# Kernel tuning notes

Measured on AMD Instinct MI355X. Metric: run time of the kernel, lower is better.

The kernel has to match this reference:

```python
import jax, jax.numpy as jnp
import numpy as np

H = 4      # heads
C = 32     # out channels per head (hidden_channels)
G = 64     # num graphs


def transformer_conv(x, src, dst, Wq, bq, Wk, bk, Wv, bv, Ws, bs):
    # PyG TransformerConv, concat=False, root_weight=True, beta=False.
    N = x.shape[0]
    q = (x @ Wq + bq).reshape(N, H, C)
    k = (x @ Wk + bk).reshape(N, H, C)
    v = (x @ Wv + bv).reshape(N, H, C)
    qe = q[dst]            # [E,H,C] gather target queries
    ke = k[src]            # [E,H,C] gather source keys
    ve = v[src]            # [E,H,C] gather source values
    alpha = (qe * ke).sum(-1) / jnp.sqrt(jnp.asarray(C, x.dtype))  # [E,H]
    amax = jax.ops.segment_max(alpha, dst, num_segments=N)          # [N,H]
    a = jnp.exp(alpha - amax[dst])
    denom = jax.ops.segment_sum(a, dst, num_segments=N)             # [N,H]
    a = a / (denom[dst] + 1e-16)
    out = jax.ops.segment_sum(ve * a[..., None], dst, num_segments=N)  # [N,H,C]
    out = out.mean(axis=1)          # concat=False -> head average
    return out + x @ Ws + bs        # root skip


def setup_inputs() -> dict:
    key = jax.random.key(0)
    ks = jax.random.split(key, 24)
    N, E, Fin = 40000, 640000, 128
    x = jax.random.normal(ks[0], (N, Fin), dtype=jnp.float32)
    edge_index = jax.random.randint(ks[1], (2, E), 0, N, dtype=jnp.int64)
    batch = jnp.sort(jax.random.randint(ks[2], (N,), 0, G, dtype=jnp.int64))
    s = 0.05
    w = lambda k, shp: jax.random.normal(k, shp, dtype=jnp.float32) * s
    d = {"x": x, "edge_index": edge_index, "batch": batch,
         "Wq1": w(ks[3], (Fin, H * C)), "bq1": w(ks[4], (H * C,)),
         "Wk1": w(ks[5], (Fin, H * C)), "bk1": w(ks[6], (H * C,)),
         "Wv1": w(ks[7], (Fin, H * C)), "bv1": w(ks[8], (H * C,)),
         "Ws1": w(ks[9], (Fin, C)), "bs1": w(ks[10], (C,)),
         "Wq2": w(ks[11], (C, H * C)), "bq2": w(ks[12], (H * C,)),
         "Wk2": w(ks[13], (C, H * C)), "bk2": w(ks[14], (H * C,)),
         "Wv2": w(ks[15], (C, H * C)), "bv2": w(ks[16], (H * C,)),
         "Ws2": w(ks[17], (C, C)), "bs2": w(ks[18], (C,)),
         "Wlin": w(ks[19], (C, 16)), "blin": w(ks[20], (16,))}
    return d


def reference(x, edge_index, batch,
              Wq1, bq1, Wk1, bk1, Wv1, bv1, Ws1, bs1,
              Wq2, bq2, Wk2, bk2, Wv2, bv2, Ws2, bs2,
              Wlin, blin):
    src, dst = edge_index[0], edge_index[1]
    h = transformer_conv(x, src, dst, Wq1, bq1, Wk1, bk1, Wv1, bv1, Ws1, bs1)
    h = jax.nn.relu(h)
    h = transformer_conv(h, src, dst, Wq2, bq2, Wk2, bk2, Wv2, bv2, Ws2, bs2)
    # global mean pool over graphs
    sums = jax.ops.segment_sum(h, batch, num_segments=G)                  # [G,C]
    cnts = jax.ops.segment_sum(jnp.ones((h.shape[0],), h.dtype), batch, num_segments=G)
    pooled = sums / jnp.maximum(cnts, 1.0)[:, None]
    return pooled @ Wlin + blin
```

## Files before the change

### kernel.cpp

```cpp
#include <hip/hip_runtime.h>
#include <hip/hip_bf16.h>
#include <hip/hip_fp16.h>
#include <math.h>

#define HH 4
#define CC 32
#define HC 128
#define GG 64

typedef _Float16 f16x2 __attribute__((ext_vector_type(2)));
typedef _Float16 f16x8 __attribute__((ext_vector_type(8)));
typedef float f32x4 __attribute__((ext_vector_type(4)));

__device__ __forceinline__ f16x2 u2h(unsigned u) {
    union { unsigned u; f16x2 h; } x; x.u = u; return x.h;
}
__device__ __forceinline__ unsigned pkh(float a, float b) {
    __half2 h = __floats2half2_rn(a, b);
    union { __half2 h; unsigned u; } x; x.h = h; return x.u;
}
__device__ __forceinline__ f16x8 uq2h8(uint4 u) {
    union { uint4 u; f16x8 h; } x; x.u = u; return x.h;
}

__device__ __forceinline__ void wfrag_item(const float* __restrict__ Wq, const float* __restrict__ Wk,
    const float* __restrict__ Wv, const float* __restrict__ Ws,
    uint4* __restrict__ wfrag, int KS, int idx)
{
    int lane = idx & 63;
    int t = idx >> 6;
    int ks = t % KS, ct = t / KS;
    int r = lane & 15, g = lane >> 4;
    const float* W; int c, stride;
    if (ct < 8)       { W = Wq; c = ct * 16 + r;        stride = HC; }
    else if (ct < 16) { W = Wk; c = (ct - 8) * 16 + r;  stride = HC; }
    else if (ct < 24) { W = Wv; c = (ct - 16) * 16 + r; stride = HC; }
    else              { W = Ws; c = (ct - 24) * 16 + r; stride = CC; }
    unsigned u[4];
    #pragma unroll
    for (int jj = 0; jj < 4; ++jj) {
        int k = ks * 32 + g * 8 + jj * 2;
        u[jj] = pkh(W[(size_t)k * stride + c], W[(size_t)(k + 1) * stride + c]);
    }
    wfrag[idx] = make_uint4(u[0], u[1], u[2], u[3]);
}

__global__ void prep_kernel(const float* __restrict__ x, unsigned* __restrict__ xh, int n4,
    const float* __restrict__ Wq1, const float* __restrict__ Wk1,
    const float* __restrict__ Wv1, const float* __restrict__ Ws1, uint4* __restrict__ wfrag1,
    const float* __restrict__ Wq2, const float* __restrict__ Wk2,
    const float* __restrict__ Wv2, const float* __restrict__ Ws2, uint4* __restrict__ wfrag2,
    int* __restrict__ deg, int N, float* __restrict__ sums)
{
    const int N1 = 26 * 4 * 64;
    const int N2 = 26 * 1 * 64;
    int i = blockIdx.x * 256 + threadIdx.x;
    if (i < n4) {
        float4 f = ((const float4*)x)[i];
        ((uint2*)xh)[i] = make_uint2(pkh(f.x, f.y), pkh(f.z, f.w));
        return;
    }
    i -= n4;
    if (i < N1) { wfrag_item(Wq1, Wk1, Wv1, Ws1, wfrag1, 4, i); return; }
    i -= N1;
    if (i < N2) { wfrag_item(Wq2, Wk2, Wv2, Ws2, wfrag2, 1, i); return; }
    i -= N2;
    if (i < N) { deg[i] = 0; return; }
    i -= N;
    if (i < GG * CC + GG) sums[i] = 0.f;
}

template<int KDIM>
__global__ __launch_bounds__(256) void qkv_mfma_kernel(
    const ushort* __restrict__ xh, const uint4* __restrict__ wfrag,
    const float* __restrict__ bq, const float* __restrict__ bk,
    const float* __restrict__ bv, const float* __restrict__ bs,
    unsigned* __restrict__ qh, uint4* __restrict__ kv4, float* __restrict__ skip,
    int N)
{
    constexpr int KS = KDIM / 32;
    const int lane = threadIdx.x & 63;
    const int wv = threadIdx.x >> 6;
    const int n0 = (blockIdx.x * 4 + wv) * 16;
    if (n0 >= N) return;
    const int r = lane & 15, g = lane >> 4;
    const int node = n0 + r;

    f16x8 a[KS];
    #pragma unroll
    for (int ks = 0; ks < KS; ++ks)
        a[ks] = uq2h8(*(const uint4*)&xh[(size_t)node * KDIM + ks * 32 + g * 8]);

    if (blockIdx.y == 0) {
        const float SC2 = 0.25500526806584186f;
        f32x4 acc[10];
        #pragma unroll
        for (int i = 0; i < 10; ++i) acc[i] = (f32x4){0.f, 0.f, 0.f, 0.f};
        #pragma unroll
        for (int i = 0; i < 8; ++i)
            #pragma unroll
            for (int ks = 0; ks < KS; ++ks) {
                f16x8 w = uq2h8(wfrag[((size_t)i * KS + ks) * 64 + lane]);
                acc[i] = __builtin_amdgcn_mfma_f32_16x16x32_f16(w, a[ks], acc[i], 0, 0, 0);
            }
        #pragma unroll
        for (int i = 0; i < 2; ++i)
            #pragma unroll
            for (int ks = 0; ks < KS; ++ks) {
                f16x8 w = uq2h8(wfrag[((size_t)(24 + i) * KS + ks) * 64 + lane]);
                acc[8 + i] = __builtin_amdgcn_mfma_f32_16x16x32_f16(w, a[ks], acc[8 + i], 0, 0, 0);
            }
        if (node < N) {
            #pragma unroll
            for (int i = 0; i < 8; ++i) {
                float4 bb = *(const float4*)&bq[i * 16 + g * 4];
                uint2 o = make_uint2(pkh((acc[i][0] + bb.x) * SC2, (acc[i][1] + bb.y) * SC2),
                                     pkh((acc[i][2] + bb.z) * SC2, (acc[i][3] + bb.w) * SC2));
                *(uint2*)&qh[(size_t)node * 64 + i * 8 + g * 2] = o;
            }
            #pragma unroll
            for (int i = 0; i < 2; ++i) {
                float4 bb = *(const float4*)&bs[i * 16 + g * 4];
                float4 o = make_float4(acc[8 + i][0] + bb.x, acc[8 + i][1] + bb.y,
                                       acc[8 + i][2] + bb.z, acc[8 + i][3] + bb.w);
                *(float4*)&skip[(size_t)node * CC + i * 16 + g * 4] = o;
            }
        }
    } else {
        f32x4 acck[8], accv[8];
        #pragma unroll
        for (int i = 0; i < 8; ++i) { acck[i] = (f32x4){0.f,0.f,0.f,0.f}; accv[i] = (f32x4){0.f,0.f,0.f,0.f}; }
        #pragma unroll
        for (int i = 0; i < 8; ++i)
            #pragma unroll
            for (int ks = 0; ks < KS; ++ks) {
                f16x8 wk = uq2h8(wfrag[((size_t)(8 + i) * KS + ks) * 64 + lane]);
                acck[i] = __builtin_amdgcn_mfma_f32_16x16x32_f16(wk, a[ks], acck[i], 0, 0, 0);
                f16x8 wvf = uq2h8(wfrag[((size_t)(16 + i) * KS + ks) * 64 + lane]);
                accv[i] = __builtin_amdgcn_mfma_f32_16x16x32_f16(wvf, a[ks], accv[i], 0, 0, 0);
            }
        if (node < N) {
            #pragma unroll
            for (int i = 0; i < 8; ++i) {
                float4 bbk = *(const float4*)&bk[i * 16 + g * 4];
                float4 bbv = *(const float4*)&bv[i * 16 + g * 4];
                uint4 o;
                o.x = pkh(acck[i][0] + bbk.x, acck[i][1] + bbk.y);
                o.y = pkh(acck[i][2] + bbk.z, acck[i][3] + bbk.w);
                o.z = pkh(accv[i][0] + bbv.x, accv[i][1] + bbv.y);
                o.w = pkh(accv[i][2] + bbv.z, accv[i][3] + bbv.w);
                kv4[(size_t)node * 32 + i * 4 + g] = o;
            }
        }
    }
}

__global__ void deg_kernel(const int* __restrict__ dst, int* __restrict__ deg, int E)
{
    int e = blockIdx.x * blockDim.x + threadIdx.x;
    if (e < E) atomicAdd(&deg[dst[e]], 1);
}

__global__ void bsum_kernel(const int* __restrict__ deg, int* __restrict__ bsum, int N)
{
    int base = blockIdx.x * 1024;
    int tid = threadIdx.x;
    int s = 0;
    for (int i = base + tid; i < base + 1024 && i < N; i += 256) s += deg[i];
    #pragma unroll
    for (int ofs = 32; ofs > 0; ofs >>= 1) s += __shfl_xor(s, ofs, 64);
    __shared__ int ws[4];
    int wid = tid >> 6;
    if ((tid & 63) == 0) ws[wid] = s;
    __syncthreads();
    if (tid == 0) bsum[blockIdx.x] = ws[0] + ws[1] + ws[2] + ws[3];
}

__global__ void bscan_kernel(int* __restrict__ bsum, int* __restrict__ off, int nb, int N)
{
    int i = threadIdx.x;
    int val = (i < nb) ? bsum[i] : 0;
    int v = val;
    #pragma unroll
    for (int ofs = 1; ofs < 64; ofs <<= 1) {
        int t = __shfl_up(v, ofs, 64);
        if (i >= ofs) v += t;
    }
    if (i < nb) bsum[i] = v - val;
    if (i == 63) off[N] = v;
}

__global__ void scan2_kernel(const int* __restrict__ deg, const int* __restrict__ bsum,
                             int* __restrict__ off, int* __restrict__ cursor, int N)
{
    int base = blockIdx.x * 1024;
    int tid = threadIdx.x;
    int idx = base + tid * 4;
    int d0 = (idx     < N) ? deg[idx]     : 0;
    int d1 = (idx + 1 < N) ? deg[idx + 1] : 0;
    int d2 = (idx + 2 < N) ? deg[idx + 2] : 0;
    int d3 = (idx + 3 < N) ? deg[idx + 3] : 0;
    int tsum = d0 + d1 + d2 + d3;
    int v = tsum;
    int lane = tid & 63;
    #pragma unroll
    for (int ofs = 1; ofs < 64; ofs <<= 1) {
        int t = __shfl_up(v, ofs, 64);
        if (lane >= ofs) v += t;
    }
    __shared__ int wsum[4];
    int wid = tid >> 6;
    if (lane == 63) wsum[wid] = v;
    __syncthreads();
    int wbase = 0;
    for (int w = 0; w < wid; ++w) wbase += wsum[w];
    int excl = bsum[blockIdx.x] + wbase + (v - tsum);
    if (idx     < N) { off[idx]     = excl;                cursor[idx]     = excl; }
    if (idx + 1 < N) { off[idx + 1] = excl + d0;           cursor[idx + 1] = excl + d0; }
    if (idx + 2 < N) { off[idx + 2] = excl + d0 + d1;      cursor[idx + 2] = excl + d0 + d1; }
    if (idx + 3 < N) { off[idx + 3] = excl + d0 + d1 + d2; cursor[idx + 3] = excl + d0 + d1 + d2; }
}

__global__ void fill_kernel(const int* __restrict__ src, const int* __restrict__ dst,
                            int* __restrict__ cursor, int* __restrict__ esrc, int E)
{
    int e = blockIdx.x * blockDim.x + threadIdx.x;
    if (e < E) {
        int d = dst[e];
        int pos = atomicAdd(&cursor[d], 1);
        esrc[pos] = src[e];
    }
}

template<int MODE>
__global__ __launch_bounds__(128) void attn_kernel(const unsigned* __restrict__ qh,
    const uint4* __restrict__ kv4, const int* __restrict__ off, const int* __restrict__ esrc,
    const float* __restrict__ skip, void* __restrict__ hout, int N)
{
    const int wave = threadIdx.x >> 6;
    const int lane = threadIdx.x & 63;
    const int n = blockIdx.x * 2 + wave;
    if (n >= N) return;
    const int half = lane >> 5;
    const int j = lane & 31;

    uint2 qv = *(const uint2*)&qh[(size_t)n * 64 + j * 2];
    f16x2 q01 = u2h(qv.x), q23 = u2h(qv.y);

    int beg = __builtin_amdgcn_readfirstlane(off[n]);
    int end = __builtin_amdgcn_readfirstlane(off[n + 1]);

    float lsum = 0.f, a0 = 0.f, a1 = 0.f, a2 = 0.f, a3 = 0.f;

    auto compute = [&](uint4 raw) {
        f16x2 k01 = u2h(raw.x), k23 = u2h(raw.y);
        f16x2 v01 = u2h(raw.z), v23 = u2h(raw.w);
#if defined(__has_builtin) && __has_builtin(__builtin_amdgcn_fdot2)
        float d = __builtin_amdgcn_fdot2(q01, k01,
                    __builtin_amdgcn_fdot2(q23, k23, 0.f, false), false);
#else
        float d = (float)q01.x*(float)k01.x + (float)q01.y*(float)k01.y
                + (float)q23.x*(float)k23.x + (float)q23.y*(float)k23.y;
#endif
        d += __shfl_xor(d, 1, 8);
        d += __shfl_xor(d, 2, 8);
        d += __shfl_xor(d, 4, 8);
        float e = exp2f(d);
        lsum += e;
        a0 = fmaf(e, (float)v01.x, a0);
        a1 = fmaf(e, (float)v01.y, a1);
        a2 = fmaf(e, (float)v23.x, a2);
        a3 = fmaf(e, (float)v23.y, a3);
    };
    auto ld = [&](int p2) -> uint4 {
        return kv4[(size_t)esrc[p2 + half] * 32 + j];
    };

    int p = beg;
    if (p + 8 <= end) {
        uint4 c0 = ld(p), c1 = ld(p + 2), c2 = ld(p + 4), c3 = ld(p + 6);
        p += 8;
        for (; p + 8 <= end; p += 8) {
            uint4 n0 = ld(p), n1 = ld(p + 2), n2 = ld(p + 4), n3 = ld(p + 6);
            compute(c0); compute(c1); compute(c2); compute(c3);
            c0 = n0; c1 = n1; c2 = n2; c3 = n3;
        }
        compute(c0); compute(c1); compute(c2); compute(c3);
    }
    for (; p < end; p += 2) {
        int idx = p + half;
        int sidx = (idx >= end) ? end - 1 : idx;
        uint4 raw = kv4[(size_t)esrc[sidx] * 32 + j];
        f16x2 k01 = u2h(raw.x), k23 = u2h(raw.y);
        f16x2 v01 = u2h(raw.z), v23 = u2h(raw.w);
#if defined(__has_builtin) && __has_builtin(__builtin_amdgcn_fdot2)
        float d = __builtin_amdgcn_fdot2(q01, k01,
                    __builtin_amdgcn_fdot2(q23, k23, 0.f, false), false);
#else
        float d = (float)q01.x*(float)k01.x + (float)q01.y*(float)k01.y
                + (float)q23.x*(float)k23.x + (float)q23.y*(float)k23.y;
#endif
        d += __shfl_xor(d, 1, 8);
        d += __shfl_xor(d, 2, 8);
        d += __shfl_xor(d, 4, 8);
        float e = exp2f(d);
        if (idx >= end) e = 0.f;
        lsum += e;
        a0 = fmaf(e, (float)v01.x, a0);
        a1 = fmaf(e, (float)v01.y, a1);
        a2 = fmaf(e, (float)v23.x, a2);
        a3 = fmaf(e, (float)v23.y, a3);
    }

    lsum += __shfl_xor(lsum, 32);
    a0 += __shfl_xor(a0, 32);
    a1 += __shfl_xor(a1, 32);
    a2 += __shfl_xor(a2, 32);
    a3 += __shfl_xor(a3, 32);

    float inv = 1.f / (lsum + 1e-16f);
    float r0 = a0 * inv, r1 = a1 * inv, r2 = a2 * inv, r3 = a3 * inv;
    r0 += __shfl_xor(r0, 8, 32);  r0 += __shfl_xor(r0, 16, 32);
    r1 += __shfl_xor(r1, 8, 32);  r1 += __shfl_xor(r1, 16, 32);
    r2 += __shfl_xor(r2, 8, 32);  r2 += __shfl_xor(r2, 16, 32);
    r3 += __shfl_xor(r3, 8, 32);  r3 += __shfl_xor(r3, 16, 32);

    if (lane < 8) {
        float4 sk = *(const float4*)&skip[(size_t)n * CC + lane * 4];
        float o0 = 0.25f * r0 + sk.x;
        float o1 = 0.25f * r1 + sk.y;
        float o2 = 0.25f * r2 + sk.z;
        float o3 = 0.25f * r3 + sk.w;
        if (MODE) {
            o0 = fmaxf(o0, 0.f); o1 = fmaxf(o1, 0.f);
            o2 = fmaxf(o2, 0.f); o3 = fmaxf(o3, 0.f);
            *(uint2*)&((unsigned*)hout)[(size_t)n * 16 + lane * 2] =
                make_uint2(pkh(o0, o1), pkh(o2, o3));
        } else {
            *(float4*)&((float*)hout)[(size_t)n * CC + lane * 4] =
                make_float4(o0, o1, o2, o3);
        }
    }
}

__global__ void pool_kernel(const float* __restrict__ h, const int* __restrict__ batch,
    float* __restrict__ sums, float* __restrict__ cntf, int N)
{
    int c = threadIdx.x & 31;
    int tn = threadIdx.x >> 5;
    int n0 = blockIdx.x * 256;
    int nend = (n0 + 256 < N) ? n0 + 256 : N;
    float acc = 0.f, cnt = 0.f;
    int curg = -1;
    for (int n = n0 + tn; n < nend; n += 8) {
        int g = batch[n];
        if (g != curg) {
            if (curg >= 0) {
                unsafeAtomicAdd(&sums[curg * CC + c], acc);
                if (c == 0) unsafeAtomicAdd(&cntf[curg], cnt);
            }
            acc = 0.f; cnt = 0.f; curg = g;
        }
        acc += h[(size_t)n * CC + c];
        cnt += 1.f;
    }
    if (curg >= 0) {
        unsafeAtomicAdd(&sums[curg * CC + c], acc);
        if (c == 0) unsafeAtomicAdd(&cntf[curg], cnt);
    }
}

__global__ void final_lin_kernel(const float* __restrict__ sums, const float* __restrict__ cntf,
    const float* __restrict__ Wlin, const float* __restrict__ blin, float* __restrict__ out)
{
    int g = blockIdx.x;
    int j = threadIdx.x;
    float cnt = fmaxf(cntf[g], 1.0f);
    float acc = 0.f;
    #pragma unroll
    for (int c = 0; c < CC; ++c)
        acc += (sums[g * CC + c] / cnt) * Wlin[c * 16 + j];
    out[g * 16 + j] = acc + blin[j];
}

extern "C" void kernel_launch(void* const* d_in, const int* in_sizes, int n_in,
                              void* d_out, int out_size, void* d_ws, size_t ws_size,
                              hipStream_t stream) {
    const float* x     = (const float*)d_in[0];
    const int*   ei    = (const int*)d_in[1];
    const int*   batch = (const int*)d_in[2];
    const float* Wq1 = (const float*)d_in[3],  *bq1 = (const float*)d_in[4];
    const float* Wk1 = (const float*)d_in[5],  *bk1 = (const float*)d_in[6];
    const float* Wv1 = (const float*)d_in[7],  *bv1 = (const float*)d_in[8];
    const float* Ws1 = (const float*)d_in[9],  *bs1 = (const float*)d_in[10];
    const float* Wq2 = (const float*)d_in[11], *bq2 = (const float*)d_in[12];
    const float* Wk2 = (const float*)d_in[13], *bk2 = (const float*)d_in[14];
    const float* Wv2 = (const float*)d_in[15], *bv2 = (const float*)d_in[16];
    const float* Ws2 = (const float*)d_in[17], *bs2 = (const float*)d_in[18];
    const float* Wlin = (const float*)d_in[19], *blin = (const float*)d_in[20];

    const int N = in_sizes[0] / 128;
    const int E = in_sizes[1] / 2;
    const int* src = ei;
    const int* dstp = ei + E;
    const int NB = (N + 1023) / 1024;
    const int Npad = (N + 63) & ~63;

    char* wp = (char*)d_ws;
    auto alloc = [&](size_t bytes) -> void* {
        void* p = wp;
        wp += (bytes + 255) & ~(size_t)255;
        return p;
    };
    unsigned* qh   = (unsigned*)alloc((size_t)N * 64 * 4);
    uint4* kv4     = (uint4*)alloc((size_t)N * 32 * 16);
    float* skip    = (float*)alloc((size_t)N * CC * 4);
    unsigned* h1h  = (unsigned*)alloc((size_t)Npad * 16 * 4);
    float* h2      = (float*)alloc((size_t)N * CC * 4);
    ushort* xh     = (ushort*)alloc((size_t)Npad * HC * 2);
    uint4* wfrag1  = (uint4*)alloc((size_t)26 * 4 * 64 * 16);
    uint4* wfrag2  = (uint4*)alloc((size_t)26 * 1 * 64 * 16);
    int* deg    = (int*)alloc((size_t)N * 4);
    int* off    = (int*)alloc((size_t)(N + 1) * 4);
    int* cursor = (int*)alloc((size_t)N * 4);
    int* esrc   = (int*)alloc((size_t)E * 4);
    int* bsum   = (int*)alloc((size_t)((NB + 63) & ~63) * 4);
    float* sums = (float*)alloc((size_t)GG * CC * 4);
    float* cntf = (float*)alloc((size_t)GG * 4);

    const int n4 = N * HC / 4;
    const int prep_total = n4 + 26 * 5 * 64 + N + GG * CC + GG;
    prep_kernel<<<(prep_total + 255) / 256, 256, 0, stream>>>(
        x, (unsigned*)xh, n4,
        Wq1, Wk1, Wv1, Ws1, wfrag1, Wq2, Wk2, Wv2, Ws2, wfrag2,
        deg, N, sums);

    deg_kernel<<<(E + 255) / 256, 256, 0, stream>>>(dstp, deg, E);
    bsum_kernel<<<NB, 256, 0, stream>>>(deg, bsum, N);
    bscan_kernel<<<1, 64, 0, stream>>>(bsum, off, NB, N);
    scan2_kernel<<<NB, 256, 0, stream>>>(deg, bsum, off, cursor, N);
    fill_kernel<<<(E + 255) / 256, 256, 0, stream>>>(src, dstp, cursor, esrc, E);

    dim3 ggrid((N + 63) / 64, 2);
    dim3 agrid((N + 1) / 2);

    qkv_mfma_kernel<128><<<ggrid, 256, 0, stream>>>(xh, wfrag1, bq1, bk1, bv1, bs1,
                                                    qh, kv4, skip, N);
    attn_kernel<1><<<agrid, 128, 0, stream>>>(qh, kv4, off, esrc, skip, h1h, N);

    qkv_mfma_kernel<32><<<ggrid, 256, 0, stream>>>((const ushort*)h1h, wfrag2, bq2, bk2, bv2, bs2,
                                                   qh, kv4, skip, N);
    attn_kernel<0><<<agrid, 128, 0, stream>>>(qh, kv4, off, esrc, skip, h2, N);

    pool_kernel<<<(N + 255) / 256, 256, 0, stream>>>(h2, batch, sums, cntf, N);
    final_lin_kernel<<<GG, 16, 0, stream>>>(sums, cntf, Wlin, blin, (float*)d_out);
}
```

Baseline: 232.1 us.

## Split QKV MFMA work into 17 single-wave output-group blocks per node tile

The QKV projection kernel now launches one 64-thread wave per 16-node tile per output group: 8 Q groups, 8 K/V groups and 1 skip group. Before, each wave computed all Q and skip, or all K and V, outputs for its tile. The goal is more parallelism and fewer live accumulators per wave, which means lower register pressure and higher occupancy. The cost is that every one of the 17 blocks reloads the same input activations, so input reads rise about 8x, and the launch has many tiny blocks.

```diff
diff --git a/kernel.cpp b/kernel.cpp
--- a/kernel.cpp
+++ b/kernel.cpp
@@ -71,7 +71,7 @@
 }
 
 template<int KDIM>
-__global__ __launch_bounds__(256) void qkv_mfma_kernel(
+__global__ __launch_bounds__(64) void qkv_mfma_kernel(
     const ushort* __restrict__ xh, const uint4* __restrict__ wfrag,
     const float* __restrict__ bq, const float* __restrict__ bk,
     const float* __restrict__ bv, const float* __restrict__ bs,
@@ -79,9 +79,9 @@
     int N)
 {
     constexpr int KS = KDIM / 32;
-    const int lane = threadIdx.x & 63;
-    const int wv = threadIdx.x >> 6;
-    const int n0 = (blockIdx.x * 4 + wv) * 16;
+    const int lane = threadIdx.x;
+    const int n0 = blockIdx.x * 16;
+    const int grp = blockIdx.y;
     if (n0 >= N) return;
     const int r = lane & 15, g = lane >> 4;
     const int node = n0 + r;
@@ -91,66 +91,58 @@
     for (int ks = 0; ks < KS; ++ks)
         a[ks] = uq2h8(*(const uint4*)&xh[(size_t)node * KDIM + ks * 32 + g * 8]);
 
-    if (blockIdx.y == 0) {
+    if (grp < 8) {
         const float SC2 = 0.25500526806584186f;
-        f32x4 acc[10];
+        f32x4 acc = (f32x4){0.f, 0.f, 0.f, 0.f};
         #pragma unroll
-        for (int i = 0; i < 10; ++i) acc[i] = (f32x4){0.f, 0.f, 0.f, 0.f};
+        for (int ks = 0; ks < KS; ++ks) {
+            f16x8 w = uq2h8(wfrag[((size_t)grp * KS + ks) * 64 + lane]);
+            acc = __builtin_amdgcn_mfma_f32_16x16x32_f16(w, a[ks], acc, 0, 0, 0);
+        }
+        if (node < N) {
+            float4 bb = *(const float4*)&bq[grp * 16 + g * 4];
+            uint2 o = make_uint2(pkh((acc[0] + bb.x) * SC2, (acc[1] + bb.y) * SC2),
+                                 pkh((acc[2] + bb.z) * SC2, (acc[3] + bb.w) * SC2));
+            *(uint2*)&qh[(size_t)node * 64 + grp * 8 + g * 2] = o;
+        }
+    } else if (grp < 16) {
+        const int i = grp - 8;
+        f32x4 acck = (f32x4){0.f, 0.f, 0.f, 0.f};
+        f32x4 accv = (f32x4){0.f, 0.f, 0.f, 0.f};
         #pragma unroll
-        for (int i = 0; i < 8; ++i)
-            #pragma unroll
-            for (int ks = 0; ks < KS; ++ks) {
-                f16x8 w = uq2h8(wfrag[((size_t)i * KS + ks) * 64 + lane]);
-                acc[i] = __builtin_amdgcn_mfma_f32_16x16x32_f16(w, a[ks], acc[i], 0, 0, 0);
-            }
+        for (int ks = 0; ks < KS; ++ks) {
+            f16x8 wk = uq2h8(wfrag[((size_t)(8 + i) * KS + ks) * 64 + lane]);
+            acck = __builtin_amdgcn_mfma_f32_16x16x32_f16(wk, a[ks], acck, 0, 0, 0);
+            f16x8 wv = uq2h8(wfrag[((size_t)(16 + i) * KS + ks) * 64 + lane]);
+            accv = __builtin_amdgcn_mfma_f32_16x16x32_f16(wv, a[ks], accv, 0, 0, 0);
+        }
+        if (node < N) {
+            float4 bbk = *(const float4*)&bk[i * 16 + g * 4];
+            float4 bbv = *(const float4*)&bv[i * 16 + g * 4];
+            uint4 o;
+            o.x = pkh(acck[0] + bbk.x, acck[1] + bbk.y);
+            o.y = pkh(acck[2] + bbk.z, acck[3] + bbk.w);
+            o.z = pkh(accv[0] + bbv.x, accv[1] + bbv.y);
+            o.w = pkh(accv[2] + bbv.z, accv[3] + bbv.w);
+            kv4[(size_t)node * 32 + i * 4 + g] = o;
+        }
+    } else {
+        f32x4 acc0 = (f32x4){0.f, 0.f, 0.f, 0.f};
+        f32x4 acc1 = (f32x4){0.f, 0.f, 0.f, 0.f};
         #pragma unroll
-        for (int i = 0; i < 2; ++i)
-            #pragma unroll
-            for (int ks = 0; ks < KS; ++ks) {
-                f16x8 w = uq2h8(wfrag[((size_t)(24 + i) * KS + ks) * 64 + lane]);
-                acc[8 + i] = __builtin_amdgcn_mfma_f32_16x16x32_f16(w, a[ks], acc[8 + i], 0, 0, 0);
-            }
+        for (int ks = 0; ks < KS; ++ks) {
+            f16x8 w0 = uq2h8(wfrag[((size_t)24 * KS + ks) * 64 + lane]);
+            acc0 = __builtin_amdgcn_mfma_f32_16x16x32_f16(w0, a[ks], acc0, 0, 0, 0);
+            f16x8 w1 = uq2h8(wfrag[((size_t)25 * KS + ks) * 64 + lane]);
+            acc1 = __builtin_amdgcn_mfma_f32_16x16x32_f16(w1, a[ks], acc1, 0, 0, 0);
+        }
         if (node < N) {
-            #pragma unroll
-            for (int i = 0; i < 8; ++i) {
-                float4 bb = *(const float4*)&bq[i * 16 + g * 4];
-                uint2 o = make_uint2(pkh((acc[i][0] + bb.x) * SC2, (acc[i][1] + bb.y) * SC2),
-                                     pkh((acc[i][2] + bb.z) * SC2, (acc[i][3] + bb.w) * SC2));
-                *(uint2*)&qh[(size_t)node * 64 + i * 8 + g * 2] = o;
-            }
-            #pragma unroll
-            for (int i = 0; i < 2; ++i) {
-                float4 bb = *(const float4*)&bs[i * 16 + g * 4];
-                float4 o = make_float4(acc[8 + i][0] + bb.x, acc[8 + i][1] + bb.y,
-                                       acc[8 + i][2] + bb.z, acc[8 + i][3] + bb.w);
-                *(float4*)&skip[(size_t)node * CC + i * 16 + g * 4] = o;
-            }
-        }
-    } else {
-        f32x4 acck[8], accv[8];
-        #pragma unroll
-        for (int i = 0; i < 8; ++i) { acck[i] = (f32x4){0.f,0.f,0.f,0.f}; accv[i] = (f32x4){0.f,0.f,0.f,0.f}; }
-        #pragma unroll
-        for (int i = 0; i < 8; ++i)
-            #pragma unroll
-            for (int ks = 0; ks < KS; ++ks) {
-                f16x8 wk = uq2h8(wfrag[((size_t)(8 + i) * KS + ks) * 64 + lane]);
-                acck[i] = __builtin_amdgcn_mfma_f32_16x16x32_f16(wk, a[ks], acck[i], 0, 0, 0);
-                f16x8 wvf = uq2h8(wfrag[((size_t)(16 + i) * KS + ks) * 64 + lane]);
-                accv[i] = __builtin_amdgcn_mfma_f32_16x16x32_f16(wvf, a[ks], accv[i], 0, 0, 0);
-            }
-        if (node < N) {
-            #pragma unroll
-            for (int i = 0; i < 8; ++i) {
-                float4 bbk = *(const float4*)&bk[i * 16 + g * 4];
-                float4 bbv = *(const float4*)&bv[i * 16 + g * 4];
-                uint4 o;
-                o.x = pkh(acck[i][0] + bbk.x, acck[i][1] + bbk.y);
-                o.y = pkh(acck[i][2] + bbk.z, acck[i][3] + bbk.w);
-                o.z = pkh(accv[i][0] + bbv.x, accv[i][1] + bbv.y);
-                o.w = pkh(accv[i][2] + bbv.z, accv[i][3] + bbv.w);
-                kv4[(size_t)node * 32 + i * 4 + g] = o;
-            }
+            float4 b0 = *(const float4*)&bs[g * 4];
+            float4 b1 = *(const float4*)&bs[16 + g * 4];
+            *(float4*)&skip[(size_t)node * CC + g * 4] =
+                make_float4(acc0[0] + b0.x, acc0[1] + b0.y, acc0[2] + b0.z, acc0[3] + b0.w);
+            *(float4*)&skip[(size_t)node * CC + 16 + g * 4] =
+                make_float4(acc1[0] + b1.x, acc1[1] + b1.y, acc1[2] + b1.z, acc1[3] + b1.w);
         }
     }
 }
@@ -441,15 +433,15 @@
     scan2_kernel<<<NB, 256, 0, stream>>>(deg, bsum, off, cursor, N);
     fill_kernel<<<(E + 255) / 256, 256, 0, stream>>>(src, dstp, cursor, esrc, E);
 
-    dim3 ggrid((N + 63) / 64, 2);
+    dim3 ggrid((N + 15) / 16, 17);
     dim3 agrid((N + 1) / 2);
 
-    qkv_mfma_kernel<128><<<ggrid, 256, 0, stream>>>(xh, wfrag1, bq1, bk1, bv1, bs1,
-                                                    qh, kv4, skip, N);
+    qkv_mfma_kernel<128><<<ggrid, 64, 0, stream>>>(xh, wfrag1, bq1, bk1, bv1, bs1,
+                                                   qh, kv4, skip, N);
     attn_kernel<1><<<agrid, 128, 0, stream>>>(qh, kv4, off, esrc, skip, h1h, N);
 
-    qkv_mfma_kernel<32><<<ggrid, 256, 0, stream>>>((const ushort*)h1h, wfrag2, bq2, bk2, bv2, bs2,
-                                                   qh, kv4, skip, N);
+    qkv_mfma_kernel<32><<<ggrid, 64, 0, stream>>>((const ushort*)h1h, wfrag2, bq2, bk2, bv2, bs2,
+                                                  qh, kv4, skip, N);
     attn_kernel<0><<<agrid, 128, 0, stream>>>(qh, kv4, off, esrc, skip, h2, N);
 
     pool_kernel<<<(N + 255) / 256, 256, 0, stream>>>(h2, batch, sums, cntf, N);
```

New measurement: 242.0 us. +4.3%, slower.
